# Kernel optimization log

Hardware: AMD Instinct MI355X
Metric: run time of the kernel (lower is better)

Reference implementation:

```python
import jax, jax.numpy as jnp
import numpy as np

EPS = 1e-3        # Sinkhorn regularization (SinkhornDistance default)
MAX_ITER = 10     # max Sinkhorn iterations
THRESH = 0.1      # early-stop threshold on |u - u_prev|
N, P, D = 8, 2048, 64


def _l2norm(x):
    # F.normalize(x, dim=-1): x / max(||x||_2, 1e-12)
    return x / jnp.maximum(jnp.linalg.norm(x, axis=-1, keepdims=True), 1e-12)


def _l1norm(x):
    # F.normalize(x, p=1, dim=-1)
    return x / jnp.maximum(jnp.sum(jnp.abs(x), axis=-1, keepdims=True), 1e-12)


def _M(C, u, v):
    # modified cost M_ij = (-C_ij + u_i + v_j) / eps
    return (-C + u[..., :, None] + v[..., None, :]) / EPS


def _sinkhorn_uv(C, mu, nu):
    """Log-domain Sinkhorn with early stopping (matches torch loop + err.item() break)."""
    u0 = jnp.zeros_like(mu)
    v0 = jnp.zeros_like(nu)

    def cond(st):
        i, u, v, err = st
        return jnp.logical_and(i < MAX_ITER, err >= THRESH)

    def body(st):
        i, u, v, _ = st
        u1 = u
        u = EPS * (jnp.log(mu + 1e-8) - jax.nn.logsumexp(_M(C, u, v), axis=-1)) + u
        # logsumexp of M^T over last dim == logsumexp of M over axis -2
        v = EPS * (jnp.log(nu + 1e-8) - jax.nn.logsumexp(_M(C, u, v), axis=-2)) + v
        err = jnp.mean(jnp.sum(jnp.abs(u - u1), axis=-1))
        return (i + 1, u, v, err)

    _, u, v, _ = jax.lax.while_loop(
        cond, body, (jnp.int32(0), u0, v0, jnp.float32(jnp.inf)))
    return u, v


def setup_inputs() -> dict:
    key = jax.random.key(0)
    ka, kb = jax.random.split(key)
    a = jax.random.normal(ka, (N, P, D), dtype=jnp.float32)
    b = jax.random.normal(kb, (N, P, D), dtype=jnp.float32)
    return {"a": a, "b": b}


def reference(a, b):
    a = _l2norm(a)
    b = _l2norm(b)
    cost = 1.0 - jnp.einsum('bnd,bmd->bnm', a, b)          # [N, P1, P2]

    # weights computed from detached cost
    Cd = jax.lax.stop_gradient(cost)
    S = 1.0 - Cd
    wa = _l1norm(jnp.clip(_l1norm(jnp.mean(S, axis=2)), 0.0))  # [N, P1]
    wb = _l1norm(jnp.clip(_l1norm(jnp.mean(S, axis=1)), 0.0))  # [N, P2]

    u, v = _sinkhorn_uv(Cd, wa, wb)
    pi = jax.lax.stop_gradient(jnp.exp(_M(Cd, u, v)))       # transport plan, detached
    D_out = jnp.sum(pi * cost, axis=(-2, -1))               # [N], reduction='none'
    return D_out
```

## Files before the change

kernel.cpp:

```cpp
#include <hip/hip_runtime.h>
#include <math.h>

#define NB 8
#define PP 2048
#define DD 64
#define EPSF 1e-3f
#define RCPE 1000.0f
#define TMAX 10
#define THRESHF 0.1f
#define NEG_INF (-1e30f)
#define QSCALE 32767.5f
#define S_DEQ  (1.0f / 32767.5f)
#define KR 512
#define KC 512
#define TSEL 0.15f

typedef __attribute__((ext_vector_type(8))) short bf16x8;
typedef __attribute__((ext_vector_type(4))) float f32x4;

__device__ __forceinline__ float waveAllMax(float v) {
#pragma unroll
    for (int m = 1; m < 64; m <<= 1) v = fmaxf(v, __shfl_xor(v, m, 64));
    return v;
}
__device__ __forceinline__ float waveAllMin(float v) {
#pragma unroll
    for (int m = 1; m < 64; m <<= 1) v = fminf(v, __shfl_xor(v, m, 64));
    return v;
}
__device__ __forceinline__ float waveAllSum(float v) {
#pragma unroll
    for (int m = 1; m < 64; m <<= 1) v += __shfl_xor(v, m, 64);
    return v;
}
__device__ __forceinline__ short f2bf(float x) {
    unsigned b = __float_as_uint(x);
    return (short)((b + 0x7FFFu + ((b >> 16) & 1u)) >> 16);
}
__device__ __forceinline__ float bf2f(short h) {
    return __uint_as_float(((unsigned)(unsigned short)h) << 16);
}

__global__ void norm_kernel(const float* __restrict__ a, const float* __restrict__ b,
                            short* __restrict__ ahi, short* __restrict__ alo,
                            short* __restrict__ bhi, short* __restrict__ blo,
                            float* __restrict__ u, float* __restrict__ v,
                            int* __restrict__ conv, float* __restrict__ out) {
    int gt = blockIdx.x * 256 + threadIdx.x;
    if (gt < NB * PP) { u[gt] = 0.0f; v[gt] = 0.0f; }
    if (gt == 0) *conv = 0;
    if (gt < NB) out[gt] = 0.0f;
    int wave = gt >> 6;
    int lane = threadIdx.x & 63;
    const float* src; short* dhi; short* dlo; int row;
    if (wave < NB * PP) { src = a; dhi = ahi; dlo = alo; row = wave; }
    else                { src = b; dhi = bhi; dlo = blo; row = wave - NB * PP; }
    float x = src[(size_t)row * DD + lane];
    float ss = waveAllSum(x * x);
    float r = 1.0f / fmaxf(sqrtf(ss), 1e-12f);
    float xn = x * r;
    short h = f2bf(xn);
    dhi[(size_t)row * DD + lane] = h;
    dlo[(size_t)row * DD + lane] = f2bf(xn - bf2f(h));
}

__global__ __launch_bounds__(256) void cost_kernel(const short* __restrict__ ahi,
        const short* __restrict__ alo, const short* __restrict__ bhi,
        const short* __restrict__ blo, unsigned short* __restrict__ C16,
        float* __restrict__ rpart, float* __restrict__ cpart,
        unsigned* __restrict__ rminp, unsigned* __restrict__ cminp) {
    __shared__ float    rsum2[256];
    __shared__ unsigned rmin2[256];
    __shared__ float    csum2[256];
    __shared__ unsigned cmin2[256];
    int b  = blockIdx.z;
    int i0 = blockIdx.y * 128;
    int j0 = blockIdx.x * 128;
    int t = threadIdx.x, w = t >> 6, lane = t & 63;
    int wi = w >> 1, wj = w & 1;
    int quad = lane >> 4, li = lane & 15;
    size_t Aoff = ((size_t)b * PP + i0 + wi * 64) * DD;
    size_t Boff = ((size_t)b * PP + j0 + wj * 64) * DD;
    f32x4 acc[4][4] = {};
#pragma unroll
    for (int kc = 0; kc < 2; ++kc) {
        int k0 = kc * 32 + quad * 8;
        bf16x8 fah[4], fal[4];
#pragma unroll
        for (int mt = 0; mt < 4; ++mt) {
            size_t o = Aoff + (size_t)(mt * 16 + li) * DD + k0;
            fah[mt] = *(const bf16x8*)(ahi + o);
            fal[mt] = *(const bf16x8*)(alo + o);
        }
#pragma unroll
        for (int nt = 0; nt < 4; ++nt) {
            size_t o = Boff + (size_t)(li * 4 + nt) * DD + k0;
            bf16x8 fbh = *(const bf16x8*)(bhi + o);
            bf16x8 fbl = *(const bf16x8*)(blo + o);
#pragma unroll
            for (int mt = 0; mt < 4; ++mt) {
                acc[mt][nt] = __builtin_amdgcn_mfma_f32_16x16x32_bf16(
                        fah[mt], fbh, acc[mt][nt], 0, 0, 0);
                acc[mt][nt] = __builtin_amdgcn_mfma_f32_16x16x32_bf16(
                        fah[mt], fbl, acc[mt][nt], 0, 0, 0);
                acc[mt][nt] = __builtin_amdgcn_mfma_f32_16x16x32_bf16(
                        fal[mt], fbh, acc[mt][nt], 0, 0, 0);
            }
        }
    }
    float csum[4] = {0.f, 0.f, 0.f, 0.f};
    unsigned cmin[4] = {0xFFFFFFFFu, 0xFFFFFFFFu, 0xFFFFFFFFu, 0xFFFFFFFFu};
#pragma unroll
    for (int mt = 0; mt < 4; ++mt) {
#pragma unroll
        for (int r = 0; r < 4; ++r) {
            int irow = wi * 64 + mt * 16 + quad * 4 + r;
            float rs = 0.0f; unsigned rm = 0xFFFFFFFFu;
            unsigned short qv[4];
#pragma unroll
            for (int nt = 0; nt < 4; ++nt) {
                int jl = wj * 64 + li * 4 + nt;
                float dot = acc[mt][nt][r];
                float cost = fminf(fmaxf(1.0f - dot, 0.0f), 2.0f);
                unsigned q = __float2uint_rn(cost * QSCALE);
                qv[nt] = (unsigned short)q;
                rs += dot;
                rm = min(rm, (q << 16) | (unsigned)(j0 + jl));
                csum[nt] += dot;
                cmin[nt] = min(cmin[nt], (q << 16) | (unsigned)(i0 + irow));
            }
            *(ushort4*)&C16[((size_t)b * PP + i0 + irow) * PP + j0 + wj * 64 + li * 4] =
                make_ushort4(qv[0], qv[1], qv[2], qv[3]);
#pragma unroll
            for (int m = 1; m < 16; m <<= 1) {
                rs += __shfl_xor(rs, m, 64);
                rm = min(rm, (unsigned)__shfl_xor((int)rm, m, 64));
            }
            if (li == 0) { rsum2[wj * 128 + irow] = rs; rmin2[wj * 128 + irow] = rm; }
        }
    }
#pragma unroll
    for (int nt = 0; nt < 4; ++nt) {
        float cv = csum[nt]; unsigned cmv = cmin[nt];
#pragma unroll
        for (int m = 16; m < 64; m <<= 1) {
            cv += __shfl_xor(cv, m, 64);
            cmv = min(cmv, (unsigned)__shfl_xor((int)cmv, m, 64));
        }
        if (quad == 0) {
            int jl = wj * 64 + li * 4 + nt;
            csum2[wi * 128 + jl] = cv; cmin2[wi * 128 + jl] = cmv;
        }
    }
    __syncthreads();
    if (t < 128) {
        rpart[(size_t)blockIdx.x * (NB * PP) + b * PP + i0 + t] = rsum2[t] + rsum2[128 + t];
        rminp[(size_t)blockIdx.x * (NB * PP) + b * PP + i0 + t] = min(rmin2[t], rmin2[128 + t]);
        cpart[(size_t)blockIdx.y * (NB * PP) + b * PP + j0 + t] = csum2[t] + csum2[128 + t];
        cminp[(size_t)blockIdx.y * (NB * PP) + b * PP + j0 + t] = min(cmin2[t], cmin2[128 + t]);
    }
}

__global__ void combine_kernel(const float* __restrict__ rpart, const float* __restrict__ cpart,
                               const unsigned* __restrict__ rminp, const unsigned* __restrict__ cminp,
                               float* __restrict__ rowS, float* __restrict__ colS,
                               unsigned* __restrict__ rowminp, unsigned* __restrict__ colminp) {
    int idx = blockIdx.x * 256 + threadIdx.x;
    float rs = 0.0f, csf = 0.0f;
    unsigned rm = 0xFFFFFFFFu, cm = 0xFFFFFFFFu;
#pragma unroll
    for (int k = 0; k < 16; ++k) {
        rs  += rpart[(size_t)k * (NB * PP) + idx];
        csf += cpart[(size_t)k * (NB * PP) + idx];
        rm = min(rm, rminp[(size_t)k * (NB * PP) + idx]);
        cm = min(cm, cminp[(size_t)k * (NB * PP) + idx]);
    }
    rowS[idx] = rs; colS[idx] = csf;
    rowminp[idx] = rm; colminp[idx] = cm;
}

__device__ __forceinline__ float blockReduceSum256(float v, float* sh) {
    v = waveAllSum(v);
    int lane = threadIdx.x & 63, w = threadIdx.x >> 6;
    if (lane == 0) sh[w] = v;
    __syncthreads();
    float r = sh[0] + sh[1] + sh[2] + sh[3];
    __syncthreads();
    return r;
}

__global__ void weights_kernel(const float* __restrict__ rowS, const float* __restrict__ colS,
                               const unsigned* __restrict__ rowminp, const unsigned* __restrict__ colminp,
                               float* __restrict__ elm, float* __restrict__ eln,
                               float* __restrict__ rowminf, float* __restrict__ colminf,
                               float* __restrict__ cthresh) {
    __shared__ float sh[4];
    int b = blockIdx.x & 7;
    bool isB = blockIdx.x >= 8;
    const float* src = (isB ? colS : rowS) + b * PP;
    float* dst = (isB ? eln : elm) + b * PP;
    int tid = threadIdx.x;
    float x[8];
    float sabs = 0.0f;
#pragma unroll
    for (int q = 0; q < 8; ++q) {
        x[q] = src[tid + q * 256] * (1.0f / (float)PP);
        sabs += fabsf(x[q]);
    }
    sabs = blockReduceSum256(sabs, sh);
    float inv1 = 1.0f / fmaxf(sabs, 1e-12f);
    float spos = 0.0f;
#pragma unroll
    for (int q = 0; q < 8; ++q) {
        x[q] = fmaxf(x[q] * inv1, 0.0f);
        spos += x[q];
    }
    spos = blockReduceSum256(spos, sh);
    float inv2 = 1.0f / fmaxf(spos, 1e-12f);
#pragma unroll
    for (int q = 0; q < 8; ++q)
        dst[tid + q * 256] = EPSF * logf(x[q] * inv2 + 1e-8f);
    if (isB) {
#pragma unroll
        for (int q = 0; q < 8; ++q) {
            int idx = b * PP + tid + q * 256;
            unsigned pc = colminp[idx];
            unsigned arg = pc & 0xffffu;
            unsigned pr = rowminp[b * PP + arg];
            float cmf = (float)(pc >> 16) * S_DEQ;
            colminf[idx] = cmf;
            cthresh[idx] = cmf - (float)(pr >> 16) * S_DEQ + TSEL;
        }
    } else {
#pragma unroll
        for (int q = 0; q < 8; ++q) {
            int idx = b * PP + tid + q * 256;
            rowminf[idx] = (float)(rowminp[idx] >> 16) * S_DEQ;
        }
    }
}

__global__ __launch_bounds__(256) void select_kernel(const unsigned short* __restrict__ C16,
        const float* __restrict__ colminf, const float* __restrict__ rowminf,
        const float* __restrict__ cthresh,
        unsigned* __restrict__ rlist, int* __restrict__ rcnt,
        unsigned* __restrict__ clist, int* __restrict__ scnt) {
    __shared__ unsigned tile32[64][36];
    __shared__ float rm_s[64];
    __shared__ unsigned lcnt[64];
    if (blockIdx.x < 4096) {
        int w = threadIdx.x >> 6, lane = threadIdx.x & 63;
        int row = blockIdx.x * 4 + w;
        int b = row >> 11;
        const uint4* cp = (const uint4*)(C16 + (size_t)row * PP);
        uint4 q4[4];
#pragma unroll
        for (int g = 0; g < 4; ++g) q4[g] = cp[g * 64 + lane];
        const float* cmb = colminf + b * PP;
        float rpmin = 1e30f;
#pragma unroll
        for (int g = 0; g < 4; ++g) {
            int jb = g * 512 + lane * 8;
            float4 cm0 = *(const float4*)(cmb + jb);
            float4 cm1 = *(const float4*)(cmb + jb + 4);
            float cm[8] = {cm0.x, cm0.y, cm0.z, cm0.w, cm1.x, cm1.y, cm1.z, cm1.w};
            unsigned qq[4] = {q4[g].x, q4[g].y, q4[g].z, q4[g].w};
#pragma unroll
            for (int h = 0; h < 4; ++h) {
                float c0 = (float)(qq[h] & 0xffffu) * S_DEQ;
                float c1 = (float)(qq[h] >> 16) * S_DEQ;
                rpmin = fminf(rpmin, fminf(c0 - cm[h * 2], c1 - cm[h * 2 + 1]));
            }
        }
        float rth = waveAllMin(rpmin) + TSEL;
        int base = 0;
#pragma unroll
        for (int g = 0; g < 4; ++g) {
            int jb = g * 512 + lane * 8;
            float4 cm0 = *(const float4*)(cmb + jb);
            float4 cm1 = *(const float4*)(cmb + jb + 4);
            float cm[8] = {cm0.x, cm0.y, cm0.z, cm0.w, cm1.x, cm1.y, cm1.z, cm1.w};
            unsigned qq[4] = {q4[g].x, q4[g].y, q4[g].z, q4[g].w};
#pragma unroll
            for (int e = 0; e < 8; ++e) {
                unsigned q = (qq[e >> 1] >> ((e & 1) * 16)) & 0xffffu;
                float cf = (float)q * S_DEQ;
                bool rq = (cf - cm[e]) <= rth;
                unsigned long long mb = __ballot(rq);
                if (rq) {
                    int pos = base + __popcll(mb & ((1ull << lane) - 1ull));
                    if (pos < KR) rlist[(size_t)row * KR + pos] = ((unsigned)(jb + e) << 16) | q;
                }
                base += __popcll(mb);
            }
        }
        if (lane == 0) rcnt[row] = base;
    } else {
        int bid = blockIdx.x - 4096;
        int b = bid >> 7;
        int rem = bid & 127;
        int j0 = (rem >> 2) * 64;
        int r0 = (rem & 3) * 512;
        int qq = rem & 3;
        int t = threadIdx.x;
        int col = t & 63, seg = t >> 6;
        float ctj = cthresh[b * PP + j0 + col];
        unsigned* mylist = clist + ((size_t)(b * PP + j0 + col)) * KC + qq * 128;
        if (t < 64) lcnt[t] = 0;
        int lrow = t >> 3, lcc = t & 7;
        uint4 pf0, pf1; float pfr = 0.0f;
        {
            const unsigned short* base0 = C16 + ((size_t)b * PP + r0 + lrow) * PP + j0;
            pf0 = ((const uint4*)base0)[lcc];
            pf1 = ((const uint4*)(base0 + (size_t)32 * PP))[lcc];
            if (t < 64) pfr = rowminf[b * PP + r0 + t];
        }
        for (int chunk = 0; chunk < 8; ++chunk) {
            *(uint4*)&tile32[lrow][lcc * 4]      = pf0;
            *(uint4*)&tile32[32 + lrow][lcc * 4] = pf1;
            if (t < 64) rm_s[t] = pfr;
            __syncthreads();
            if (chunk < 7) {
                int rn = r0 + (chunk + 1) * 64;
                const unsigned short* base0 = C16 + ((size_t)b * PP + rn + lrow) * PP + j0;
                pf0 = ((const uint4*)base0)[lcc];
                pf1 = ((const uint4*)(base0 + (size_t)32 * PP))[lcc];
                if (t < 64) pfr = rowminf[b * PP + rn + t];
            }
            int rbase = r0 + chunk * 64;
#pragma unroll
            for (int rr = 0; rr < 16; ++rr) {
                int row = seg * 16 + rr;
                unsigned w32 = tile32[row][col >> 1];
                unsigned q = (col & 1) ? (w32 >> 16) : (w32 & 0xffffu);
                float cf = (float)q * S_DEQ;
                if (cf - rm_s[row] <= ctj) {
                    unsigned pos = atomicAdd(&lcnt[col], 1u);
                    if (pos < 128) mylist[pos] = ((unsigned)(rbase + row) << 16) | q;
                }
            }
            __syncthreads();
        }
        if (t < 64)
            scnt[(b * PP + j0 + t) * 4 + qq] = min((int)lcnt[t], 128);
    }
}

__global__ __launch_bounds__(256) void u_kernel(const unsigned* __restrict__ rlist,
        const int* __restrict__ rcnt, const float* __restrict__ v,
        const float* __restrict__ elm, float* __restrict__ u, float* __restrict__ du,
        const int* __restrict__ conv) {
    if (*conv) return;
    int w = threadIdx.x >> 6, lane = threadIdx.x & 63;
    int row = blockIdx.x * 4 + w;
    int b = row >> 11;
    int cnt = min(rcnt[row], KR);
    const unsigned* lst = rlist + (size_t)row * KR;
    const float* vb = v + (b << 11);
    float x[8];
    float m = NEG_INF;
#pragma unroll
    for (int s = 0; s < 8; ++s) {
        int e = lane + s * 64;
        x[s] = NEG_INF;
        if (e < cnt) {
            unsigned wd = lst[e];
            x[s] = vb[wd >> 16] - (float)(wd & 0xffffu) * S_DEQ;
        }
        m = fmaxf(m, x[s]);
    }
    m = waveAllMax(m);
    float s = 0.0f;
#pragma unroll
    for (int k = 0; k < 8; ++k) s += __expf((x[k] - m) * RCPE);
    s = waveAllSum(s);
    if (lane == 0) {
        float un = elm[row] - m - EPSF * logf(s);
        du[row] = fabsf(un - u[row]);
        u[row] = un;
    }
}

__global__ __launch_bounds__(256) void v_kernel(const unsigned* __restrict__ clist,
        const int* __restrict__ scnt, const float* __restrict__ u,
        const float* __restrict__ eln, float* __restrict__ v,
        const float* __restrict__ du, int* __restrict__ conv) {
    if (*conv) return;
    int w = threadIdx.x >> 6, lane = threadIdx.x & 63;
    int jg = blockIdx.x * 4 + w;
    int b = jg >> 11;
    int4 sc = *(const int4*)&scnt[jg * 4];
    int cn[4] = {sc.x, sc.y, sc.z, sc.w};
    const unsigned* lst = clist + (size_t)jg * KC;
    const float* ub = u + (b << 11);
    float x[8];
    float m = NEG_INF;
#pragma unroll
    for (int s = 0; s < 8; ++s) {
        int e = lane + s * 64;
        int sg = e >> 7, k = e & 127;
        x[s] = NEG_INF;
        if (k < cn[sg]) {
            unsigned wd = lst[sg * 128 + k];
            x[s] = ub[wd >> 16] - (float)(wd & 0xffffu) * S_DEQ;
        }
        m = fmaxf(m, x[s]);
    }
    m = waveAllMax(m);
    float s = 0.0f;
#pragma unroll
    for (int k = 0; k < 8; ++k) s += __expf((x[k] - m) * RCPE);
    s = waveAllSum(s);
    if (lane == 0)
        v[jg] = eln[jg] - m - EPSF * logf(s);
    if (blockIdx.x == 0) {
        __shared__ float sh[4];
        int t = threadIdx.x;
        float sacc = 0.0f;
#pragma unroll
        for (int q = 0; q < 64; ++q) sacc += du[t + q * 256];
        sacc = waveAllSum(sacc);
        if (lane == 0) sh[w] = sacc;
        __syncthreads();
        if (t == 0) {
            float tot = sh[0] + sh[1] + sh[2] + sh[3];
            if (tot * (1.0f / (float)NB) < THRESHF) *conv = 1;
        }
    }
}

__global__ __launch_bounds__(256) void emd_kernel(const unsigned* __restrict__ rlist,
        const int* __restrict__ rcnt, const float* __restrict__ u,
        const float* __restrict__ v, float* __restrict__ epart) {
    __shared__ float sh[4];
    int w = threadIdx.x >> 6, lane = threadIdx.x & 63;
    int row = blockIdx.x * 4 + w;
    int b = row >> 11;
    int cnt = min(rcnt[row], KR);
    const unsigned* lst = rlist + (size_t)row * KR;
    const float* vb = v + (b << 11);
    float ui = u[row];
    float s = 0.0f;
#pragma unroll
    for (int k = 0; k < 8; ++k) {
        int e = lane + k * 64;
        if (e < cnt) {
            unsigned wd = lst[e];
            float cf = (float)(wd & 0xffffu) * S_DEQ;
            s += __expf((ui + vb[wd >> 16] - cf) * RCPE) * cf;
        }
    }
    s = waveAllSum(s);
    if (lane == 0) sh[w] = s;
    __syncthreads();
    if (threadIdx.x == 0) epart[blockIdx.x] = sh[0] + sh[1] + sh[2] + sh[3];
}

__global__ __launch_bounds__(256) void emd_finalize(const float* __restrict__ epart,
                                                    float* __restrict__ out) {
    __shared__ float sh[4];
    int b = blockIdx.x;
    int t = threadIdx.x;
    float s = epart[b * 512 + t] + epart[b * 512 + 256 + t];
    s = blockReduceSum256(s, sh);
    if (t == 0) out[b] = s;
}

extern "C" void kernel_launch(void* const* d_in, const int* in_sizes, int n_in,
                              void* d_out, int out_size, void* d_ws, size_t ws_size,
                              hipStream_t stream) {
    const float* a = (const float*)d_in[0];
    const float* b = (const float*)d_in[1];
    float* out = (float*)d_out;

    const size_t MBs = 1024ull * 1024ull;
    char* ws = (char*)d_ws;
    unsigned short* C16 = (unsigned short*)ws;
    short* ahi   = (short*)(ws + 64 * MBs);
    short* alo   = (short*)(ws + 66 * MBs);
    short* bhi   = (short*)(ws + 68 * MBs);
    short* blo   = (short*)(ws + 70 * MBs);
    float* rpart = (float*)(ws + 72 * MBs);
    float* cpart = (float*)(ws + 73 * MBs);
    unsigned* rminp = (unsigned*)(ws + 74 * MBs);
    unsigned* cminp = (unsigned*)(ws + 75 * MBs);
    unsigned* rlist = (unsigned*)(ws + 64 * MBs);
    unsigned* clist = (unsigned*)(ws + 96 * MBs);
    char* tail = ws + 128 * MBs;
    size_t off = 0;
    const size_t szV = (size_t)NB * PP * 4;
    int*   scnt    = (int*)(tail + off); off += (size_t)NB * PP * 4 * 4;
    float* rowS    = (float*)(tail + off); off += szV;
    float* colS    = (float*)(tail + off); off += szV;
    unsigned* rowminp = (unsigned*)(tail + off); off += szV;
    unsigned* colminp = (unsigned*)(tail + off); off += szV;
    float* rowminf = (float*)(tail + off); off += szV;
    float* colminf = (float*)(tail + off); off += szV;
    float* cthresh = (float*)(tail + off); off += szV;
    float* elm     = (float*)(tail + off); off += szV;
    float* eln     = (float*)(tail + off); off += szV;
    float* u       = (float*)(tail + off); off += szV;
    float* v       = (float*)(tail + off); off += szV;
    float* du      = (float*)(tail + off); off += szV;
    int*   rcnt    = (int*)(tail + off); off += szV;
    int*   conv    = (int*)(tail + off); off += 64;
    float* epart   = rowS;
    if (ws_size < 128 * MBs + off) return;

    norm_kernel<<<(2 * NB * PP) / 4, 256, 0, stream>>>(a, b, ahi, alo, bhi, blo,
            u, v, conv, out);
    cost_kernel<<<dim3(PP / 128, PP / 128, NB), 256, 0, stream>>>(
            ahi, alo, bhi, blo, C16, rpart, cpart, rminp, cminp);
    combine_kernel<<<64, 256, 0, stream>>>(rpart, cpart, rminp, cminp,
            rowS, colS, rowminp, colminp);
    weights_kernel<<<16, 256, 0, stream>>>(rowS, colS, rowminp, colminp,
            elm, eln, rowminf, colminf, cthresh);
    select_kernel<<<4096 + 1024, 256, 0, stream>>>(C16, colminf, rowminf,
            cthresh, rlist, rcnt, clist, scnt);
    for (int it = 0; it < TMAX; ++it) {
        u_kernel<<<NB * PP / 4, 256, 0, stream>>>(rlist, rcnt, v, elm, u, du, conv);
        v_kernel<<<NB * PP / 4, 256, 0, stream>>>(clist, scnt, u, eln, v, du, conv);
    }
    emd_kernel<<<NB * PP / 4, 256, 0, stream>>>(rlist, rcnt, u, v, epart);
    emd_finalize<<<NB, 256, 0, stream>>>(epart, out);
}
```

Baseline: 349.1 us.

## Compute cost row/column means via summed-vector dot products and shrink cost tiles

Row and column means of the similarity matrix are now computed algebraically: a new kernel sums the normalized vectors per batch, and the weights kernel takes a dot product of each row with the other side's sum vector. This removes the per-tile row/column sum reductions and the partial-sum buffers from the cost kernel. The cost kernel tile also shrinks to 128x64 per block with 32 rows per wave, which doubles the grid and the row-min partials the combine step has to merge. The weights kernel now reads every normalized vector with only 16 blocks, which may make it bandwidth- or latency-bound.

After: 362.6 us. 3.9% more time.

```diff
diff --git a/kernel.cpp b/kernel.cpp
--- a/kernel.cpp
+++ b/kernel.cpp
@@ -45,11 +45,13 @@
                             short* __restrict__ ahi, short* __restrict__ alo,
                             short* __restrict__ bhi, short* __restrict__ blo,
                             float* __restrict__ u, float* __restrict__ v,
-                            int* __restrict__ conv, float* __restrict__ out) {
+                            int* __restrict__ conv, float* __restrict__ out,
+                            float* __restrict__ Sa) {
     int gt = blockIdx.x * 256 + threadIdx.x;
     if (gt < NB * PP) { u[gt] = 0.0f; v[gt] = 0.0f; }
     if (gt == 0) *conv = 0;
     if (gt < NB) out[gt] = 0.0f;
+    if (gt < 2 * NB * DD) Sa[gt] = 0.0f;
     int wave = gt >> 6;
     int lane = threadIdx.x & 63;
     const float* src; short* dhi; short* dlo; int row;
@@ -64,30 +66,60 @@
     dlo[(size_t)row * DD + lane] = f2bf(xn - bf2f(h));
 }
 
+__global__ void sumvec_kernel(const short* __restrict__ ahi, const short* __restrict__ alo,
+                              const short* __restrict__ bhi, const short* __restrict__ blo,
+                              float* __restrict__ Sa, float* __restrict__ Sb) {
+    int b = blockIdx.x >> 3;
+    bool isB = (blockIdx.x >> 2) & 1;
+    int qtr = blockIdx.x & 3;
+    const short* hi = (isB ? bhi : ahi) + ((size_t)b * PP + qtr * 512) * DD;
+    const short* lo = (isB ? blo : alo) + ((size_t)b * PP + qtr * 512) * DD;
+    float* dst = (isB ? Sb : Sa) + b * DD;
+    int t = threadIdx.x;
+    int w = t >> 6, lane = t & 63;
+    int rl = lane >> 3, dq = lane & 7;
+    float s[8] = {};
+#pragma unroll
+    for (int it = 0; it < 16; ++it) {
+        size_t o = (size_t)(w * 128 + it * 8 + rl) * DD + dq * 8;
+        bf16x8 h = *(const bf16x8*)(hi + o);
+        bf16x8 l = *(const bf16x8*)(lo + o);
+#pragma unroll
+        for (int e = 0; e < 8; ++e) s[e] += bf2f(h[e]) + bf2f(l[e]);
+    }
+#pragma unroll
+    for (int e = 0; e < 8; ++e) {
+#pragma unroll
+        for (int m = 8; m < 64; m <<= 1) s[e] += __shfl_xor(s[e], m, 64);
+    }
+    __shared__ float sh[4][64];
+    if (rl == 0) {
+#pragma unroll
+        for (int e = 0; e < 8; ++e) sh[w][dq * 8 + e] = s[e];
+    }
+    __syncthreads();
+    if (t < 64) atomicAdd(&dst[t], sh[0][t] + sh[1][t] + sh[2][t] + sh[3][t]);
+}
+
 __global__ __launch_bounds__(256) void cost_kernel(const short* __restrict__ ahi,
         const short* __restrict__ alo, const short* __restrict__ bhi,
         const short* __restrict__ blo, unsigned short* __restrict__ C16,
-        float* __restrict__ rpart, float* __restrict__ cpart,
         unsigned* __restrict__ rminp, unsigned* __restrict__ cminp) {
-    __shared__ float    rsum2[256];
-    __shared__ unsigned rmin2[256];
-    __shared__ float    csum2[256];
-    __shared__ unsigned cmin2[256];
+    __shared__ unsigned cmin2[4][64];
     int b  = blockIdx.z;
     int i0 = blockIdx.y * 128;
-    int j0 = blockIdx.x * 128;
+    int j0 = blockIdx.x * 64;
     int t = threadIdx.x, w = t >> 6, lane = t & 63;
-    int wi = w >> 1, wj = w & 1;
     int quad = lane >> 4, li = lane & 15;
-    size_t Aoff = ((size_t)b * PP + i0 + wi * 64) * DD;
-    size_t Boff = ((size_t)b * PP + j0 + wj * 64) * DD;
-    f32x4 acc[4][4] = {};
+    size_t Aoff = ((size_t)b * PP + i0 + w * 32) * DD;
+    size_t Boff = ((size_t)b * PP + j0) * DD;
+    f32x4 acc[2][4] = {};
 #pragma unroll
     for (int kc = 0; kc < 2; ++kc) {
         int k0 = kc * 32 + quad * 8;
-        bf16x8 fah[4], fal[4];
-#pragma unroll
-        for (int mt = 0; mt < 4; ++mt) {
+        bf16x8 fah[2], fal[2];
+#pragma unroll
+        for (int mt = 0; mt < 2; ++mt) {
             size_t o = Aoff + (size_t)(mt * 16 + li) * DD + k0;
             fah[mt] = *(const bf16x8*)(ahi + o);
             fal[mt] = *(const bf16x8*)(alo + o);
@@ -98,7 +130,7 @@
             bf16x8 fbh = *(const bf16x8*)(bhi + o);
             bf16x8 fbl = *(const bf16x8*)(blo + o);
 #pragma unroll
-            for (int mt = 0; mt < 4; ++mt) {
+            for (int mt = 0; mt < 2; ++mt) {
                 acc[mt][nt] = __builtin_amdgcn_mfma_f32_16x16x32_bf16(
                         fah[mt], fbh, acc[mt][nt], 0, 0, 0);
                 acc[mt][nt] = __builtin_amdgcn_mfma_f32_16x16x32_bf16(
@@ -108,74 +140,56 @@
             }
         }
     }
-    float csum[4] = {0.f, 0.f, 0.f, 0.f};
     unsigned cmin[4] = {0xFFFFFFFFu, 0xFFFFFFFFu, 0xFFFFFFFFu, 0xFFFFFFFFu};
 #pragma unroll
-    for (int mt = 0; mt < 4; ++mt) {
+    for (int mt = 0; mt < 2; ++mt) {
 #pragma unroll
         for (int r = 0; r < 4; ++r) {
-            int irow = wi * 64 + mt * 16 + quad * 4 + r;
-            float rs = 0.0f; unsigned rm = 0xFFFFFFFFu;
+            int irow = w * 32 + mt * 16 + quad * 4 + r;
+            unsigned rm = 0xFFFFFFFFu;
             unsigned short qv[4];
 #pragma unroll
             for (int nt = 0; nt < 4; ++nt) {
-                int jl = wj * 64 + li * 4 + nt;
                 float dot = acc[mt][nt][r];
                 float cost = fminf(fmaxf(1.0f - dot, 0.0f), 2.0f);
                 unsigned q = __float2uint_rn(cost * QSCALE);
                 qv[nt] = (unsigned short)q;
-                rs += dot;
-                rm = min(rm, (q << 16) | (unsigned)(j0 + jl));
-                csum[nt] += dot;
+                rm = min(rm, (q << 16) | (unsigned)(j0 + li * 4 + nt));
                 cmin[nt] = min(cmin[nt], (q << 16) | (unsigned)(i0 + irow));
             }
-            *(ushort4*)&C16[((size_t)b * PP + i0 + irow) * PP + j0 + wj * 64 + li * 4] =
+            *(ushort4*)&C16[((size_t)b * PP + i0 + irow) * PP + j0 + li * 4] =
                 make_ushort4(qv[0], qv[1], qv[2], qv[3]);
 #pragma unroll
-            for (int m = 1; m < 16; m <<= 1) {
-                rs += __shfl_xor(rs, m, 64);
+            for (int m = 1; m < 16; m <<= 1)
                 rm = min(rm, (unsigned)__shfl_xor((int)rm, m, 64));
-            }
-            if (li == 0) { rsum2[wj * 128 + irow] = rs; rmin2[wj * 128 + irow] = rm; }
+            if (li == 0)
+                rminp[(size_t)blockIdx.x * (NB * PP) + b * PP + i0 + irow] = rm;
         }
     }
 #pragma unroll
     for (int nt = 0; nt < 4; ++nt) {
-        float cv = csum[nt]; unsigned cmv = cmin[nt];
-#pragma unroll
-        for (int m = 16; m < 64; m <<= 1) {
-            cv += __shfl_xor(cv, m, 64);
-            cmv = min(cmv, (unsigned)__shfl_xor((int)cmv, m, 64));
-        }
-        if (quad == 0) {
-            int jl = wj * 64 + li * 4 + nt;
-            csum2[wi * 128 + jl] = cv; cmin2[wi * 128 + jl] = cmv;
-        }
+        unsigned cmv = cmin[nt];
+        cmv = min(cmv, (unsigned)__shfl_xor((int)cmv, 16, 64));
+        cmv = min(cmv, (unsigned)__shfl_xor((int)cmv, 32, 64));
+        if (quad == 0) cmin2[w][li * 4 + nt] = cmv;
     }
     __syncthreads();
-    if (t < 128) {
-        rpart[(size_t)blockIdx.x * (NB * PP) + b * PP + i0 + t] = rsum2[t] + rsum2[128 + t];
-        rminp[(size_t)blockIdx.x * (NB * PP) + b * PP + i0 + t] = min(rmin2[t], rmin2[128 + t]);
-        cpart[(size_t)blockIdx.y * (NB * PP) + b * PP + j0 + t] = csum2[t] + csum2[128 + t];
-        cminp[(size_t)blockIdx.y * (NB * PP) + b * PP + j0 + t] = min(cmin2[t], cmin2[128 + t]);
-    }
-}
-
-__global__ void combine_kernel(const float* __restrict__ rpart, const float* __restrict__ cpart,
-                               const unsigned* __restrict__ rminp, const unsigned* __restrict__ cminp,
-                               float* __restrict__ rowS, float* __restrict__ colS,
+    if (t < 64)
+        cminp[(size_t)blockIdx.y * (NB * PP) + b * PP + j0 + t] =
+            min(min(cmin2[0][t], cmin2[1][t]), min(cmin2[2][t], cmin2[3][t]));
+}
+
+__global__ void combine_kernel(const unsigned* __restrict__ rminp,
+                               const unsigned* __restrict__ cminp,
                                unsigned* __restrict__ rowminp, unsigned* __restrict__ colminp) {
     int idx = blockIdx.x * 256 + threadIdx.x;
-    float rs = 0.0f, csf = 0.0f;
     unsigned rm = 0xFFFFFFFFu, cm = 0xFFFFFFFFu;
 #pragma unroll
-    for (int k = 0; k < 16; ++k) {
-        rs  += rpart[(size_t)k * (NB * PP) + idx];
-        csf += cpart[(size_t)k * (NB * PP) + idx];
+    for (int k = 0; k < 32; ++k)
         rm = min(rm, rminp[(size_t)k * (NB * PP) + idx]);
+#pragma unroll
+    for (int k = 0; k < 16; ++k)
         cm = min(cm, cminp[(size_t)k * (NB * PP) + idx]);
-    }
-    rowS[idx] = rs; colS[idx] = csf;
     rowminp[idx] = rm; colminp[idx] = cm;
 }
 
@@ -189,22 +203,39 @@
     return r;
 }
 
-__global__ void weights_kernel(const float* __restrict__ rowS, const float* __restrict__ colS,
+__global__ void weights_kernel(const float* __restrict__ Sa, const float* __restrict__ Sb,
+                               const short* __restrict__ ahi, const short* __restrict__ alo,
+                               const short* __restrict__ bhi, const short* __restrict__ blo,
                                const unsigned* __restrict__ rowminp, const unsigned* __restrict__ colminp,
                                float* __restrict__ elm, float* __restrict__ eln,
                                float* __restrict__ rowminf, float* __restrict__ colminf,
                                float* __restrict__ cthresh) {
     __shared__ float sh[4];
+    __shared__ float sv[64];
     int b = blockIdx.x & 7;
     bool isB = blockIdx.x >= 8;
-    const float* src = (isB ? colS : rowS) + b * PP;
+    const short* hi = (isB ? bhi : ahi) + (size_t)b * PP * DD;
+    const short* lo = (isB ? blo : alo) + (size_t)b * PP * DD;
+    const float* svecg = (isB ? Sa : Sb) + b * DD;
     float* dst = (isB ? eln : elm) + b * PP;
     int tid = threadIdx.x;
+    if (tid < 64) sv[tid] = svecg[tid];
+    __syncthreads();
     float x[8];
     float sabs = 0.0f;
 #pragma unroll
     for (int q = 0; q < 8; ++q) {
-        x[q] = src[tid + q * 256] * (1.0f / (float)PP);
+        int row = tid + q * 256;
+        float dot = 0.0f;
+#pragma unroll
+        for (int dq = 0; dq < 8; ++dq) {
+            bf16x8 h = *(const bf16x8*)(hi + (size_t)row * DD + dq * 8);
+            bf16x8 l = *(const bf16x8*)(lo + (size_t)row * DD + dq * 8);
+#pragma unroll
+            for (int e = 0; e < 8; ++e)
+                dot += (bf2f(h[e]) + bf2f(l[e])) * sv[dq * 8 + e];
+        }
+        x[q] = dot * (1.0f / (float)PP);
         sabs += fabsf(x[q]);
     }
     sabs = blockReduceSum256(sabs, sh);
@@ -480,18 +511,14 @@
     short* alo   = (short*)(ws + 66 * MBs);
     short* bhi   = (short*)(ws + 68 * MBs);
     short* blo   = (short*)(ws + 70 * MBs);
-    float* rpart = (float*)(ws + 72 * MBs);
-    float* cpart = (float*)(ws + 73 * MBs);
-    unsigned* rminp = (unsigned*)(ws + 74 * MBs);
-    unsigned* cminp = (unsigned*)(ws + 75 * MBs);
+    unsigned* rminp = (unsigned*)(ws + 72 * MBs);
+    unsigned* cminp = (unsigned*)(ws + 74 * MBs);
     unsigned* rlist = (unsigned*)(ws + 64 * MBs);
     unsigned* clist = (unsigned*)(ws + 96 * MBs);
     char* tail = ws + 128 * MBs;
     size_t off = 0;
     const size_t szV = (size_t)NB * PP * 4;
     int*   scnt    = (int*)(tail + off); off += (size_t)NB * PP * 4 * 4;
-    float* rowS    = (float*)(tail + off); off += szV;
-    float* colS    = (float*)(tail + off); off += szV;
     unsigned* rowminp = (unsigned*)(tail + off); off += szV;
     unsigned* colminp = (unsigned*)(tail + off); off += szV;
     float* rowminf = (float*)(tail + off); off += szV;
@@ -503,18 +530,20 @@
     float* v       = (float*)(tail + off); off += szV;
     float* du      = (float*)(tail + off); off += szV;
     int*   rcnt    = (int*)(tail + off); off += szV;
+    float* Sa      = (float*)(tail + off); off += (size_t)2 * NB * DD * 4;
+    float* Sb      = Sa + NB * DD;
+    float* epart   = (float*)(tail + off); off += (size_t)NB * PP / 4 * 4;
     int*   conv    = (int*)(tail + off); off += 64;
-    float* epart   = rowS;
     if (ws_size < 128 * MBs + off) return;
 
     norm_kernel<<<(2 * NB * PP) / 4, 256, 0, stream>>>(a, b, ahi, alo, bhi, blo,
-            u, v, conv, out);
-    cost_kernel<<<dim3(PP / 128, PP / 128, NB), 256, 0, stream>>>(
-            ahi, alo, bhi, blo, C16, rpart, cpart, rminp, cminp);
-    combine_kernel<<<64, 256, 0, stream>>>(rpart, cpart, rminp, cminp,
-            rowS, colS, rowminp, colminp);
-    weights_kernel<<<16, 256, 0, stream>>>(rowS, colS, rowminp, colminp,
-            elm, eln, rowminf, colminf, cthresh);
+            u, v, conv, out, Sa);
+    sumvec_kernel<<<64, 256, 0, stream>>>(ahi, alo, bhi, blo, Sa, Sb);
+    cost_kernel<<<dim3(PP / 64, PP / 128, NB), 256, 0, stream>>>(
+            ahi, alo, bhi, blo, C16, rminp, cminp);
+    combine_kernel<<<64, 256, 0, stream>>>(rminp, cminp, rowminp, colminp);
+    weights_kernel<<<16, 256, 0, stream>>>(Sa, Sb, ahi, alo, bhi, blo,
+            rowminp, colminp, elm, eln, rowminf, colminf, cthresh);
     select_kernel<<<4096 + 1024, 256, 0, stream>>>(C16, colminf, rowminf,
             cthresh, rlist, rcnt, clist, scnt);
     for (int it = 0; it < TMAX; ++it) {
```
